# Optimization experiments

Measured on AMD Instinct MI355X. Metric: run time of the kernel, lower is better.

## Reference

```python
import jax, jax.numpy as jnp
import numpy as np

N_NODES = 40000
N_EDGES = 640000
D_FEAT = 128


def setup_inputs() -> dict:
    key = jax.random.key(0)
    k1, k2, k3, k4, k5 = jax.random.split(key, 5)
    x = jax.random.normal(k1, (N_NODES, D_FEAT), dtype=jnp.float32)
    edge_rows = jax.random.randint(k2, (N_EDGES,), 0, N_NODES, dtype=jnp.int32)
    edge_cols = jax.random.randint(k3, (N_EDGES,), 0, N_NODES, dtype=jnp.int32)
    adj_vals = jax.random.uniform(k4, (N_EDGES,), dtype=jnp.float32)
    bias = jax.random.normal(k5, (D_FEAT,), dtype=jnp.float32)
    return {"x": x, "edge_rows": edge_rows, "edge_cols": edge_cols,
            "adj_vals": adj_vals, "bias": bias}


def reference(x, edge_rows, edge_cols, adj_vals, bias):
    # SpMM: out[r] = sum_e adj_vals[e] * x[edge_cols[e]] for edges with row r
    msgs = adj_vals[:, None] * x[edge_cols]                    # [E, D]
    agg = jax.ops.segment_sum(msgs, edge_rows, num_segments=N_NODES)  # [E,D]->[N,D]
    # degree = sparse row-sum of adj values
    deg = jax.ops.segment_sum(adj_vals, edge_rows, num_segments=N_NODES)  # [N]
    deg = deg[:, None]
    # mean aggregation; rows with zero degree give NaN in torch, masked to 0
    out = jnp.where(deg == 0, 0.0, agg / jnp.where(deg == 0, 1.0, deg))
    return out + bias
```

## Files before the change

kernel.cpp:

```cpp
#include <hip/hip_runtime.h>

#define N_NODES 40000
#define N_EDGES 640000
#define D_FEAT  128
#define CAP     32
#define OCAP    8192
#define NSLICE  8
#define SLICE_NODES 5000
#define GROUPS  250
#define CHUNK   2560
#define EPT     10
#define SCAT_BLOCKS (GROUPS * NSLICE)
#define CONV_BLOCKS 5000
#define SCAN_BLOCK 256
#define N_SCAN_BLOCKS ((N_NODES + SCAN_BLOCK - 1) / SCAN_BLOCK)

typedef float    f32x4 __attribute__((ext_vector_type(4)));
typedef unsigned u32x4 __attribute__((ext_vector_type(4)));

__device__ __forceinline__ unsigned bf16r(float f) {
    unsigned u = __float_as_uint(f);
    return (u + 0x7FFFu + ((u >> 16) & 1u)) >> 16;
}


__global__ __launch_bounds__(256) void prep_kernel(
    const float* __restrict__ x,
    const int*   __restrict__ rows,
    const int*   __restrict__ cols,
    const float* __restrict__ vals,
    int*          __restrict__ cursors,
    unsigned*     __restrict__ bucket,
    int2*         __restrict__ overflow,
    uint2*        __restrict__ xbf)
{
    int b = blockIdx.x;
    if (b < SCAT_BLOCKS) {
        int grp  = b >> 3;
        int sl   = b & 7;
        int base = grp * CHUNK;
        int rlo  = sl * SLICE_NODES;
        int rhi  = rlo + SLICE_NODES;
        #pragma unroll
        for (int i = 0; i < EPT; ++i) {
            int e = base + i * 256 + threadIdx.x;
            int r = rows[e];
            if (r >= rlo && r < rhi) {
                unsigned p = ((unsigned)cols[e] << 16) | bf16r(vals[e]);
                int slot = atomicAdd(&cursors[r], 1);
                if (slot < CAP) bucket[(size_t)r * CAP + slot] = p;
                else { int o = atomicAdd(&cursors[N_NODES], 1);
                       if (o < OCAP) overflow[o] = make_int2(r, (int)p); }
            }
        }
        return;
    }
    int idx = (b - SCAT_BLOCKS) * 256 + threadIdx.x;
    float4 f = ((const float4*)x)[idx];
    uint2 o;
    o.x = bf16r(f.x) | (bf16r(f.y) << 16);
    o.y = bf16r(f.z) | (bf16r(f.w) << 16);
    xbf[idx] = o;
}

__global__ __launch_bounds__(256) void gather_bf_kernel(
    const uint2*    __restrict__ xbf,
    const int*      __restrict__ cursors,
    const unsigned* __restrict__ bucket,
    const int2*     __restrict__ overflow,
    const float*    __restrict__ bias,
    float*          __restrict__ out)
{
    int b    = blockIdx.x;
    int hw   = threadIdx.x >> 5;
    int lane = threadIdx.x & 31;
    int node = (b & 7) * SLICE_NODES + (b >> 3) * 8 + hw;

    int k = min(cursors[node], CAP);
    const unsigned* base = bucket + (size_t)node * CAP;

    unsigned ent = (lane < k) ? base[lane] : 0xFFFFFFFFu;

    #pragma unroll
    for (int kk = 2; kk <= 32; kk <<= 1) {
        #pragma unroll
        for (int j = kk >> 1; j > 0; j >>= 1) {
            unsigned other = __shfl_xor(ent, j, 64);
            bool up      = ((lane & kk) == 0);
            bool lower   = ((lane & j) == 0);
            unsigned mn  = min(ent, other), mx = max(ent, other);
            ent = (up == lower) ? mn : mx;
        }
    }

    int wb = threadIdx.x & 32;

    float4 acc0 = make_float4(0.f, 0.f, 0.f, 0.f);
    float4 acc1 = make_float4(0.f, 0.f, 0.f, 0.f);
    float  deg  = 0.f;

    #define PROC(entry, acc)  {                                            \
        unsigned _en = (entry);                                            \
        float _v = __uint_as_float(_en << 16);                             \
        unsigned _c = _en >> 16;                                           \
        uint2 _w = xbf[(size_t)_c * 32 + lane];                            \
        float _f0 = __uint_as_float(_w.x << 16);                           \
        float _f1 = __uint_as_float(_w.x & 0xFFFF0000u);                   \
        float _f2 = __uint_as_float(_w.y << 16);                           \
        float _f3 = __uint_as_float(_w.y & 0xFFFF0000u);                   \
        deg += _v;                                                         \
        acc.x += _v * _f0; acc.y += _v * _f1;                              \
        acc.z += _v * _f2; acc.w += _v * _f3; }

    int e = 0;
    for (; e + 4 <= k; e += 4) {
        unsigned p0 = __shfl(ent, wb + e,     64);
        unsigned p1 = __shfl(ent, wb + e + 1, 64);
        unsigned p2 = __shfl(ent, wb + e + 2, 64);
        unsigned p3 = __shfl(ent, wb + e + 3, 64);
        PROC(p0, acc0); PROC(p1, acc1); PROC(p2, acc0); PROC(p3, acc1);
    }
    for (; e < k; ++e) {
        unsigned p = __shfl(ent, wb + e, 64);
        PROC(p, acc0);
    }

    int oc = min(cursors[N_NODES], OCAP);
    for (int i = 0; i < oc; ++i) {
        int2 entv = overflow[i];
        if (entv.x == node) PROC((unsigned)entv.y, acc0);
    }
    #undef PROC

    float inv = (deg == 0.f) ? 0.f : 1.f / deg;
    float4 bv = ((const float4*)bias)[lane];
    f32x4 ov;
    ov.x = (acc0.x + acc1.x) * inv + bv.x;
    ov.y = (acc0.y + acc1.y) * inv + bv.y;
    ov.z = (acc0.z + acc1.z) * inv + bv.z;
    ov.w = (acc0.w + acc1.w) * inv + bv.w;
    __builtin_nontemporal_store(ov, (f32x4*)(out + (size_t)node * D_FEAT) + lane);
}


__global__ __launch_bounds__(256) void histogram_kernel(
    const int* __restrict__ rows, int* __restrict__ counts)
{
    int e = blockIdx.x * blockDim.x + threadIdx.x;
    if (e < N_EDGES) atomicAdd(&counts[rows[e]], 1);
}

__global__ __launch_bounds__(SCAN_BLOCK) void scan1_kernel(
    const int* __restrict__ counts, int* __restrict__ offsets, int* __restrict__ blocksums)
{
    __shared__ int tmp[SCAN_BLOCK];
    int t = threadIdx.x;
    int g = blockIdx.x * SCAN_BLOCK + t;
    int v = (g < N_NODES) ? counts[g] : 0;
    tmp[t] = v;
    __syncthreads();
    #pragma unroll
    for (int off = 1; off < SCAN_BLOCK; off <<= 1) {
        int add = (t >= off) ? tmp[t - off] : 0;
        __syncthreads();
        tmp[t] += add;
        __syncthreads();
    }
    if (g < N_NODES) offsets[g] = tmp[t] - v;
    if (t == SCAN_BLOCK - 1) blocksums[blockIdx.x] = tmp[t];
}

__global__ __launch_bounds__(SCAN_BLOCK) void scan2_kernel(int* __restrict__ blocksums)
{
    __shared__ int tmp[SCAN_BLOCK];
    int t = threadIdx.x;
    int v = (t < N_SCAN_BLOCKS) ? blocksums[t] : 0;
    tmp[t] = v;
    __syncthreads();
    #pragma unroll
    for (int off = 1; off < SCAN_BLOCK; off <<= 1) {
        int add = (t >= off) ? tmp[t - off] : 0;
        __syncthreads();
        tmp[t] += add;
        __syncthreads();
    }
    if (t < N_SCAN_BLOCKS) blocksums[t] = tmp[t] - v;
}

__global__ __launch_bounds__(SCAN_BLOCK) void scan3_kernel(
    int* __restrict__ offsets, int* __restrict__ cursors, const int* __restrict__ blocksums)
{
    int t = threadIdx.x;
    int g = blockIdx.x * SCAN_BLOCK + t;
    if (g < N_NODES) {
        int o = offsets[g] + blocksums[blockIdx.x];
        offsets[g] = o;
        cursors[g] = o;
    }
    if (g == 0) offsets[N_NODES] = N_EDGES;
}

__global__ __launch_bounds__(256) void bucket_kernel(
    const int* __restrict__ rows, const int* __restrict__ cols,
    const float* __restrict__ vals, int* __restrict__ cursors, int2* __restrict__ bucket)
{
    int e = blockIdx.x * blockDim.x + threadIdx.x;
    if (e >= N_EDGES) return;
    int r = rows[e];
    int pos = atomicAdd(&cursors[r], 1);
    bucket[pos] = make_int2(cols[e], __float_as_int(vals[e]));
}

__global__ __launch_bounds__(256) void gather_csr_kernel(
    const float* __restrict__ x, const int* __restrict__ offsets,
    const int2* __restrict__ bucket, const float* __restrict__ bias,
    float* __restrict__ out)
{
    int t = blockIdx.x * blockDim.x + threadIdx.x;
    int node = t >> 5;
    if (node >= N_NODES) return;
    int lane = t & 31;
    int beg = offsets[node];
    int end = offsets[node + 1];
    float4 acc = make_float4(0.f, 0.f, 0.f, 0.f);
    float deg = 0.f;
    int2 ent = (beg < end) ? bucket[beg] : make_int2(0, 0);
    for (int e = beg; e < end; ++e) {
        int2 cur = ent;
        if (e + 1 < end) ent = bucket[e + 1];
        float v = __int_as_float(cur.y);
        deg += v;
        float4 xv = ((const float4*)(x + (size_t)cur.x * D_FEAT))[lane];
        acc.x += v * xv.x; acc.y += v * xv.y; acc.z += v * xv.z; acc.w += v * xv.w;
    }
    float inv = (deg == 0.f) ? 0.f : 1.f / deg;
    float4 bv = ((const float4*)bias)[lane];
    float4 ov;
    ov.x = acc.x * inv + bv.x; ov.y = acc.y * inv + bv.y;
    ov.z = acc.z * inv + bv.z; ov.w = acc.w * inv + bv.w;
    ((float4*)(out + (size_t)node * D_FEAT))[lane] = ov;
}


__global__ __launch_bounds__(256) void edge_scatter_kernel(
    const float* __restrict__ x, const int* __restrict__ rows,
    const int* __restrict__ cols, const float* __restrict__ vals,
    float* __restrict__ agg, float* __restrict__ deg)
{
    int t = blockIdx.x * blockDim.x + threadIdx.x;
    int edge = t >> 5;
    if (edge >= N_EDGES) return;
    int lane = t & 31;
    int row = rows[edge]; int col = cols[edge]; float v = vals[edge];
    float4 xv = ((const float4*)(x + (size_t)col * D_FEAT))[lane];
    float* dst = agg + (size_t)row * D_FEAT + lane * 4;
    unsafeAtomicAdd(dst + 0, v * xv.x);
    unsafeAtomicAdd(dst + 1, v * xv.y);
    unsafeAtomicAdd(dst + 2, v * xv.z);
    unsafeAtomicAdd(dst + 3, v * xv.w);
    if (lane == 0) unsafeAtomicAdd(deg + row, v);
}

__global__ __launch_bounds__(256) void finalize_kernel(
    float* __restrict__ out, const float* __restrict__ deg, const float* __restrict__ bias)
{
    int t = blockIdx.x * blockDim.x + threadIdx.x;
    int node = t >> 5;
    if (node >= N_NODES) return;
    int lane = t & 31;
    float d = deg[node];
    float inv = (d == 0.f) ? 0.f : 1.f / d;
    float4* o = (float4*)(out + (size_t)node * D_FEAT) + lane;
    float4 bv = ((const float4*)bias)[lane];
    float4 ov = *o;
    ov.x = ov.x * inv + bv.x; ov.y = ov.y * inv + bv.y;
    ov.z = ov.z * inv + bv.z; ov.w = ov.w * inv + bv.w;
    *o = ov;
}


extern "C" void kernel_launch(void* const* d_in, const int* in_sizes, int n_in,
                              void* d_out, int out_size, void* d_ws, size_t ws_size,
                              hipStream_t stream) {
    const float* x    = (const float*)d_in[0];
    const int*   rows = (const int*)  d_in[1];
    const int*   cols = (const int*)  d_in[2];
    const float* vals = (const float*)d_in[3];
    const float* bias = (const float*)d_in[4];
    float* out = (float*)d_out;

    char* wb = (char*)d_ws;
    int*      f_cursors  = (int*)     wb;
    int2*     f_overflow = (int2*)   (wb + 160128);
    uint2*    f_xbf      = (uint2*)  (wb + 225792);
    unsigned* f_bucket   = (unsigned*)(wb + 10465792);
    size_t need_fast = 10465792 + (size_t)N_NODES * CAP * 4;

    int* w = (int*)d_ws;
    size_t need_csr = ((size_t)120448 + 2u * N_EDGES) * sizeof(int);

    if (ws_size >= need_fast) {
        (void)hipMemsetAsync(f_cursors, 0, (size_t)(N_NODES + 1) * 4, stream);
        prep_kernel<<<SCAT_BLOCKS + CONV_BLOCKS, 256, 0, stream>>>(
            x, rows, cols, vals, f_cursors, f_bucket, f_overflow, f_xbf);
        gather_bf_kernel<<<N_NODES / 8, 256, 0, stream>>>(
            f_xbf, f_cursors, f_bucket, f_overflow, bias, out);
    } else if (ws_size >= need_csr) {
        int*  counts    = w;
        int*  offsets   = w + 40064;
        int*  cursors   = w + 80128;
        int*  blocksums = w + 120128;
        int2* bucket    = (int2*)(w + 120448);
        (void)hipMemsetAsync(counts, 0, N_NODES * sizeof(int), stream);
        histogram_kernel<<<(N_EDGES + 255) / 256, 256, 0, stream>>>(rows, counts);
        scan1_kernel<<<N_SCAN_BLOCKS, SCAN_BLOCK, 0, stream>>>(counts, offsets, blocksums);
        scan2_kernel<<<1, SCAN_BLOCK, 0, stream>>>(blocksums);
        scan3_kernel<<<N_SCAN_BLOCKS, SCAN_BLOCK, 0, stream>>>(offsets, cursors, blocksums);
        bucket_kernel<<<(N_EDGES + 255) / 256, 256, 0, stream>>>(rows, cols, vals, cursors, bucket);
        int threads = N_NODES * 32;
        gather_csr_kernel<<<(threads + 255) / 256, 256, 0, stream>>>(x, offsets, bucket, bias, out);
    } else {
        float* deg = (float*)d_ws;
        (void)hipMemsetAsync(out, 0, (size_t)N_NODES * D_FEAT * sizeof(float), stream);
        (void)hipMemsetAsync(deg, 0, (size_t)N_NODES * sizeof(float), stream);
        int et = N_EDGES * 32;
        edge_scatter_kernel<<<(et + 255) / 256, 256, 0, stream>>>(x, rows, cols, vals, out, deg);
        int nt = N_NODES * 32;
        finalize_kernel<<<(nt + 255) / 256, 256, 0, stream>>>(out, deg, bias);
    }
}
```

Measured before the change: 134.7 us.

## Fuse memset, scatter, convert and gather into one cooperative persistent kernel

Replaces the memset plus two kernel launches with a single cooperative kernel of 1024 persistent blocks that zeroes the cursors, scatters edges into buckets, converts x to bf16, and gathers, using grid-wide syncs between phases. The goal is to remove launch overhead and inter-kernel gaps. In exchange it adds grid.sync costs and grid-stride loops, and it caps parallelism at 1024 blocks. It also depends on all 1024 blocks being co-resident, otherwise the cooperative launch fails and is silently ignored.

```diff
diff --git a/kernel.cpp b/kernel.cpp
--- a/kernel.cpp
+++ b/kernel.cpp
@@ -1,4 +1,7 @@
 #include <hip/hip_runtime.h>
+#include <hip/hip_cooperative_groups.h>
+
+namespace cg = cooperative_groups;
 
 #define N_NODES 40000
 #define N_EDGES 640000
@@ -10,8 +13,9 @@
 #define GROUPS  250
 #define CHUNK   2560
 #define EPT     10
-#define SCAT_BLOCKS (GROUPS * NSLICE)
-#define CONV_BLOCKS 5000
+#define SCAT_UNITS (GROUPS * NSLICE)
+#define FUSE_BLOCKS 1024
+#define FUSE_THREADS (FUSE_BLOCKS * 256)
 #define SCAN_BLOCK 256
 #define N_SCAN_BLOCKS ((N_NODES + SCAN_BLOCK - 1) / SCAN_BLOCK)
 
@@ -24,7 +28,7 @@
 }
 
 
-__global__ __launch_bounds__(256) void prep_kernel(
+__global__ __launch_bounds__(256) void fused_kernel(
     const float* __restrict__ x,
     const int*   __restrict__ rows,
     const int*   __restrict__ cols,
@@ -32,12 +36,19 @@
     int*          __restrict__ cursors,
     unsigned*     __restrict__ bucket,
     int2*         __restrict__ overflow,
-    uint2*        __restrict__ xbf)
-{
-    int b = blockIdx.x;
-    if (b < SCAT_BLOCKS) {
-        int grp  = b >> 3;
-        int sl   = b & 7;
+    uint2*        __restrict__ xbf,
+    const float*  __restrict__ bias,
+    float*        __restrict__ out)
+{
+    cg::grid_group grid = cg::this_grid();
+    int tid = blockIdx.x * 256 + threadIdx.x;
+
+    for (int i = tid; i <= N_NODES; i += FUSE_THREADS) cursors[i] = 0;
+    grid.sync();
+
+    for (int u = blockIdx.x; u < SCAT_UNITS; u += FUSE_BLOCKS) {
+        int sl   = u & 7;
+        int grp  = u >> 3;
         int base = grp * CHUNK;
         int rlo  = sl * SLICE_NODES;
         int rhi  = rlo + SLICE_NODES;
@@ -53,93 +64,88 @@
                        if (o < OCAP) overflow[o] = make_int2(r, (int)p); }
             }
         }
-        return;
-    }
-    int idx = (b - SCAT_BLOCKS) * 256 + threadIdx.x;
-    float4 f = ((const float4*)x)[idx];
-    uint2 o;
-    o.x = bf16r(f.x) | (bf16r(f.y) << 16);
-    o.y = bf16r(f.z) | (bf16r(f.w) << 16);
-    xbf[idx] = o;
-}
-
-__global__ __launch_bounds__(256) void gather_bf_kernel(
-    const uint2*    __restrict__ xbf,
-    const int*      __restrict__ cursors,
-    const unsigned* __restrict__ bucket,
-    const int2*     __restrict__ overflow,
-    const float*    __restrict__ bias,
-    float*          __restrict__ out)
-{
-    int b    = blockIdx.x;
+    }
+
+    for (int i = tid; i < N_NODES * 32; i += FUSE_THREADS) {
+        float4 f = ((const float4*)x)[i];
+        uint2 o;
+        o.x = bf16r(f.x) | (bf16r(f.y) << 16);
+        o.y = bf16r(f.z) | (bf16r(f.w) << 16);
+        xbf[i] = o;
+    }
+
+    grid.sync();
+
     int hw   = threadIdx.x >> 5;
     int lane = threadIdx.x & 31;
-    int node = (b & 7) * SLICE_NODES + (b >> 3) * 8 + hw;
-
-    int k = min(cursors[node], CAP);
-    const unsigned* base = bucket + (size_t)node * CAP;
-
-    unsigned ent = (lane < k) ? base[lane] : 0xFFFFFFFFu;
-
-    #pragma unroll
-    for (int kk = 2; kk <= 32; kk <<= 1) {
+    int wb   = threadIdx.x & 32;
+    int oc   = min(cursors[N_NODES], OCAP);
+
+    for (int ng = blockIdx.x; ng < N_NODES / 8; ng += FUSE_BLOCKS) {
+        int node = (ng & 7) * SLICE_NODES + (ng >> 3) * 8 + hw;
+
+        int k = min(cursors[node], CAP);
+        const unsigned* base = bucket + (size_t)node * CAP;
+
+        unsigned ent = (lane < k) ? base[lane] : 0xFFFFFFFFu;
+
         #pragma unroll
-        for (int j = kk >> 1; j > 0; j >>= 1) {
-            unsigned other = __shfl_xor(ent, j, 64);
-            bool up      = ((lane & kk) == 0);
-            bool lower   = ((lane & j) == 0);
-            unsigned mn  = min(ent, other), mx = max(ent, other);
-            ent = (up == lower) ? mn : mx;
-        }
-    }
-
-    int wb = threadIdx.x & 32;
-
-    float4 acc0 = make_float4(0.f, 0.f, 0.f, 0.f);
-    float4 acc1 = make_float4(0.f, 0.f, 0.f, 0.f);
-    float  deg  = 0.f;
-
-    #define PROC(entry, acc)  {                                            \
-        unsigned _en = (entry);                                            \
-        float _v = __uint_as_float(_en << 16);                             \
-        unsigned _c = _en >> 16;                                           \
-        uint2 _w = xbf[(size_t)_c * 32 + lane];                            \
-        float _f0 = __uint_as_float(_w.x << 16);                           \
-        float _f1 = __uint_as_float(_w.x & 0xFFFF0000u);                   \
-        float _f2 = __uint_as_float(_w.y << 16);                           \
-        float _f3 = __uint_as_float(_w.y & 0xFFFF0000u);                   \
-        deg += _v;                                                         \
-        acc.x += _v * _f0; acc.y += _v * _f1;                              \
-        acc.z += _v * _f2; acc.w += _v * _f3; }
-
-    int e = 0;
-    for (; e + 4 <= k; e += 4) {
-        unsigned p0 = __shfl(ent, wb + e,     64);
-        unsigned p1 = __shfl(ent, wb + e + 1, 64);
-        unsigned p2 = __shfl(ent, wb + e + 2, 64);
-        unsigned p3 = __shfl(ent, wb + e + 3, 64);
-        PROC(p0, acc0); PROC(p1, acc1); PROC(p2, acc0); PROC(p3, acc1);
-    }
-    for (; e < k; ++e) {
-        unsigned p = __shfl(ent, wb + e, 64);
-        PROC(p, acc0);
-    }
-
-    int oc = min(cursors[N_NODES], OCAP);
-    for (int i = 0; i < oc; ++i) {
-        int2 entv = overflow[i];
-        if (entv.x == node) PROC((unsigned)entv.y, acc0);
-    }
-    #undef PROC
-
-    float inv = (deg == 0.f) ? 0.f : 1.f / deg;
-    float4 bv = ((const float4*)bias)[lane];
-    f32x4 ov;
-    ov.x = (acc0.x + acc1.x) * inv + bv.x;
-    ov.y = (acc0.y + acc1.y) * inv + bv.y;
-    ov.z = (acc0.z + acc1.z) * inv + bv.z;
-    ov.w = (acc0.w + acc1.w) * inv + bv.w;
-    __builtin_nontemporal_store(ov, (f32x4*)(out + (size_t)node * D_FEAT) + lane);
+        for (int kk = 2; kk <= 32; kk <<= 1) {
+            #pragma unroll
+            for (int j = kk >> 1; j > 0; j >>= 1) {
+                unsigned other = __shfl_xor(ent, j, 64);
+                bool up    = ((lane & kk) == 0);
+                bool lower = ((lane & j) == 0);
+                unsigned mn = min(ent, other), mx = max(ent, other);
+                ent = (up == lower) ? mn : mx;
+            }
+        }
+
+        float4 acc0 = make_float4(0.f, 0.f, 0.f, 0.f);
+        float4 acc1 = make_float4(0.f, 0.f, 0.f, 0.f);
+        float  deg  = 0.f;
+
+        #define PROC(entry, acc)  {                                        \
+            unsigned _en = (entry);                                        \
+            float _v = __uint_as_float(_en << 16);                         \
+            unsigned _c = _en >> 16;                                       \
+            uint2 _w = xbf[(size_t)_c * 32 + lane];                        \
+            float _f0 = __uint_as_float(_w.x << 16);                       \
+            float _f1 = __uint_as_float(_w.x & 0xFFFF0000u);               \
+            float _f2 = __uint_as_float(_w.y << 16);                       \
+            float _f3 = __uint_as_float(_w.y & 0xFFFF0000u);               \
+            deg += _v;                                                     \
+            acc.x += _v * _f0; acc.y += _v * _f1;                          \
+            acc.z += _v * _f2; acc.w += _v * _f3; }
+
+        int e = 0;
+        for (; e + 4 <= k; e += 4) {
+            unsigned p0 = __shfl(ent, wb + e,     64);
+            unsigned p1 = __shfl(ent, wb + e + 1, 64);
+            unsigned p2 = __shfl(ent, wb + e + 2, 64);
+            unsigned p3 = __shfl(ent, wb + e + 3, 64);
+            PROC(p0, acc0); PROC(p1, acc1); PROC(p2, acc0); PROC(p3, acc1);
+        }
+        for (; e < k; ++e) {
+            unsigned p = __shfl(ent, wb + e, 64);
+            PROC(p, acc0);
+        }
+
+        for (int i = 0; i < oc; ++i) {
+            int2 entv = overflow[i];
+            if (entv.x == node) PROC((unsigned)entv.y, acc0);
+        }
+        #undef PROC
+
+        float inv = (deg == 0.f) ? 0.f : 1.f / deg;
+        float4 bv = ((const float4*)bias)[lane];
+        f32x4 ov;
+        ov.x = (acc0.x + acc1.x) * inv + bv.x;
+        ov.y = (acc0.y + acc1.y) * inv + bv.y;
+        ov.z = (acc0.z + acc1.z) * inv + bv.z;
+        ov.w = (acc0.w + acc1.w) * inv + bv.w;
+        __builtin_nontemporal_store(ov, (f32x4*)(out + (size_t)node * D_FEAT) + lane);
+    }
 }
 
 
@@ -300,11 +306,14 @@
     size_t need_csr = ((size_t)120448 + 2u * N_EDGES) * sizeof(int);
 
     if (ws_size >= need_fast) {
-        (void)hipMemsetAsync(f_cursors, 0, (size_t)(N_NODES + 1) * 4, stream);
-        prep_kernel<<<SCAT_BLOCKS + CONV_BLOCKS, 256, 0, stream>>>(
-            x, rows, cols, vals, f_cursors, f_bucket, f_overflow, f_xbf);
-        gather_bf_kernel<<<N_NODES / 8, 256, 0, stream>>>(
-            f_xbf, f_cursors, f_bucket, f_overflow, bias, out);
+        void* args[] = {
+            (void*)&x, (void*)&rows, (void*)&cols, (void*)&vals,
+            (void*)&f_cursors, (void*)&f_bucket, (void*)&f_overflow,
+            (void*)&f_xbf, (void*)&bias, (void*)&out
+        };
+        (void)hipLaunchCooperativeKernel((void*)fused_kernel,
+                                         dim3(FUSE_BLOCKS), dim3(256),
+                                         args, 0, stream);
     } else if (ws_size >= need_csr) {
         int*  counts    = w;
         int*  offsets   = w + 40064;
```

Result: slower. 332.2 us (+146.6%).
